# Optimization experiments

Measured on AMD Instinct MI355X. Metric: run time of the kernel, lower is better.

## Reference

```python
import jax, jax.numpy as jnp
import numpy as np

D_MODEL = 1024
NUM_HEADS = 16

def _dense_params(key, d_in, d_out):
    kw, _ = jax.random.split(key)
    # flax default: lecun_normal kernel, zeros bias
    W = jax.random.normal(kw, (d_in, d_out), dtype=jnp.float32) / np.sqrt(d_in)
    b = jnp.zeros((d_out,), dtype=jnp.float32)
    return W, b

def setup_inputs() -> dict:
    key = jax.random.key(0)
    ks = jax.random.split(key, 8)
    B, Tx, Tc = 2, 2048, 2048
    x = jax.random.normal(ks[0], (B, Tx, D_MODEL), dtype=jnp.float32)
    context = jax.random.normal(ks[1], (B, Tc, D_MODEL), dtype=jnp.float32)
    Wq, bq = _dense_params(ks[2], D_MODEL, D_MODEL)
    Wks, bks = _dense_params(ks[3], D_MODEL, D_MODEL)
    Wvs, bvs = _dense_params(ks[4], D_MODEL, D_MODEL)
    Wkc, bkc = _dense_params(ks[5], D_MODEL, D_MODEL)
    Wvc, bvc = _dense_params(ks[6], D_MODEL, D_MODEL)
    Wo, bo = _dense_params(ks[7], D_MODEL, D_MODEL)
    return {"x": x, "context": context,
            "Wq": Wq, "bq": bq, "Wks": Wks, "bks": bks, "Wvs": Wvs, "bvs": bvs,
            "Wkc": Wkc, "bkc": bkc, "Wvc": Wvc, "bvc": bvc, "Wo": Wo, "bo": bo}

def _split_heads(t, H):
    B, T, C = t.shape
    return t.reshape(B, T, H, C // H).transpose(0, 2, 1, 3)  # [B,H,T,hd]

def reference(x, context, Wq, bq, Wks, bks, Wvs, bvs, Wkc, bkc, Wvc, bvc, Wo, bo):
    H = NUM_HEADS
    head_dim = D_MODEL // H
    q = x @ Wq + bq
    k = jnp.concatenate([x @ Wks + bks, context @ Wkc + bkc], axis=1)
    v = jnp.concatenate([x @ Wvs + bvs, context @ Wvc + bvc], axis=1)
    q = _split_heads(q, H)  # [B,H,Tq,hd]
    k = _split_heads(k, H)  # [B,H,Tk,hd]
    v = _split_heads(v, H)
    attn = jnp.einsum('bhqd,bhkd->bhqk', q, k) / jnp.sqrt(jnp.float32(head_dim))
    attn = jax.nn.softmax(attn, axis=-1)
    out = jnp.einsum('bhqk,bhkd->bhqd', attn, v)
    B, _, Tq, _ = out.shape
    out = out.transpose(0, 2, 1, 3).reshape(B, Tq, D_MODEL)
    return out @ Wo + bo
```

## Files before the change

### kernel.cpp

```cpp
#include <hip/hip_runtime.h>
#include <hip/hip_bf16.h>
#include <math.h>


typedef _Float16 f16;
typedef _Float16 f16x8 __attribute__((ext_vector_type(8)));
typedef _Float16 f16x4v __attribute__((ext_vector_type(4)));
typedef float    f32x4 __attribute__((ext_vector_type(4)));

#define MFMA_F16(a, b, c) __builtin_amdgcn_mfma_f32_16x16x32_f16((a), (b), (c), 0, 0, 0)

__device__ __forceinline__ void glds16(const f16* g, f16* l) {
    __builtin_amdgcn_global_load_lds(
        (const __attribute__((address_space(1))) void*)g,
        (__attribute__((address_space(3))) void*)l, 16, 0, 0);
}

__global__ __launch_bounds__(256) void convert_xc(
    const float4* __restrict__ x, const float4* __restrict__ ctx,
    f16x4v* __restrict__ xb, f16x4v* __restrict__ cb)
{
    const int n4 = (2 * 2048 * 1024) / 4;
    int i = blockIdx.x * 256 + threadIdx.x;
    float4 v;
    f16x4v* dst;
    if (i < n4) { v = x[i];        dst = xb + i; }
    else        { v = ctx[i - n4]; dst = cb + (i - n4); }
    f16x4v h = { (f16)v.x, (f16)v.y, (f16)v.z, (f16)v.w };
    *dst = h;
}

__global__ __launch_bounds__(256) void pack_w(
    const float* __restrict__ W0, const float* __restrict__ W1,
    const float* __restrict__ W2, const float* __restrict__ W3,
    const float* __restrict__ W4, const float* __restrict__ W5,
    f16* __restrict__ out)
{
    const float* Ws[6] = { W0, W1, W2, W3, W4, W5 };
    const float* W = Ws[blockIdx.z];
    f16* Wt = out + (size_t)blockIdx.z * (1024 * 1024);

    __shared__ float tile[32][33];
    const int tx = threadIdx.x & 31, ty = threadIdx.x >> 5;
    const int n0 = blockIdx.x * 32, k0 = blockIdx.y * 32;

#pragma unroll
    for (int i = 0; i < 4; ++i) {
        int r = i * 8 + ty;
        tile[r][tx] = W[(size_t)(k0 + r) * 1024 + n0 + tx];
    }
    __syncthreads();
#pragma unroll
    for (int i = 0; i < 4; ++i) {
        int r = i * 8 + ty;
        Wt[(size_t)(n0 + r) * 1024 + k0 + tx] = (f16)tile[tx][r];
    }
}

template <typename OutT>
__device__ __forceinline__ void gemm_128x128(
    const f16* __restrict__ A, const f16* __restrict__ Bt,
    const float* __restrict__ bias, OutT* __restrict__ out,
    int row_stride, int row_off)
{
    __shared__ alignas(16) f16 As[128 * 32];
    __shared__ alignas(16) f16 Bs[128 * 32];

    const int m0 = blockIdx.x * 128, n0 = blockIdx.y * 128;
    const int tid = threadIdx.x;
    const int w = tid >> 6, lane = tid & 63, quad = lane >> 4, l15 = lane & 15;
    const int wm = (w >> 1) * 64, wn = (w & 1) * 64;

    const int r0 = tid >> 2, ch0 = (tid & 3) * 8;
    f16* as0 = &As[(w * 64) * 8];
    f16* as1 = &As[(256 + w * 64) * 8];
    f16* bs0 = &Bs[(w * 64) * 8];
    f16* bs1 = &Bs[(256 + w * 64) * 8];

    f32x4 acc[4][4] = {};

    for (int k0 = 0; k0 < 1024; k0 += 32) {
        glds16(&A[(size_t)(m0 + r0) * 1024 + k0 + ch0], as0);
        glds16(&A[(size_t)(m0 + 64 + r0) * 1024 + k0 + ch0], as1);
        glds16(&Bt[(size_t)(n0 + r0) * 1024 + k0 + ch0], bs0);
        glds16(&Bt[(size_t)(n0 + 64 + r0) * 1024 + k0 + ch0], bs1);
        __syncthreads();

        f16x8 a[4], b[4];
#pragma unroll
        for (int i = 0; i < 4; ++i) a[i] = *(const f16x8*)&As[(wm + i * 16 + l15) * 32 + quad * 8];
#pragma unroll
        for (int i = 0; i < 4; ++i) b[i] = *(const f16x8*)&Bs[(wn + i * 16 + l15) * 32 + quad * 8];

#pragma unroll
        for (int mi = 0; mi < 4; ++mi)
#pragma unroll
            for (int ni = 0; ni < 4; ++ni)
                acc[mi][ni] = MFMA_F16(a[mi], b[ni], acc[mi][ni]);
        __syncthreads();
    }

#pragma unroll
    for (int mi = 0; mi < 4; ++mi) {
#pragma unroll
        for (int r = 0; r < 4; ++r) {
            int row = m0 + wm + mi * 16 + quad * 4 + r;
            int orow = (row >> 11) * row_stride + row_off + (row & 2047);
#pragma unroll
            for (int ni = 0; ni < 4; ++ni) {
                int col = n0 + wn + ni * 16 + l15;
                out[(size_t)orow * 1024 + col] = (OutT)(acc[mi][ni][r] + bias[col]);
            }
        }
    }
}

__global__ __launch_bounds__(256) void proj_gemm(
    const f16* __restrict__ xb, const f16* __restrict__ cb,
    const f16* __restrict__ wt,
    const float* __restrict__ bq, const float* __restrict__ bks,
    const float* __restrict__ bvs, const float* __restrict__ bkc,
    const float* __restrict__ bvc,
    f16* __restrict__ qbuf, f16* __restrict__ kbuf, f16* __restrict__ vbuf)
{
    const int z = blockIdx.z;
    const f16* A = (z <= 2) ? xb : cb;
    const f16* Bt = wt + (size_t)z * (1024 * 1024);
    const float* bias = (z == 0) ? bq : (z == 1) ? bks : (z == 2) ? bvs
                       : (z == 3) ? bkc : bvc;
    f16* out = (z == 0) ? qbuf : (z == 1 || z == 3) ? kbuf : vbuf;
    const int row_stride = (z == 0) ? 2048 : 4096;
    const int row_off = (z >= 3) ? 2048 : 0;
    gemm_128x128<f16>(A, Bt, bias, out, row_stride, row_off);
}

__global__ __launch_bounds__(256) void out_gemm(
    const f16* __restrict__ abuf, const f16* __restrict__ wt_o,
    const float* __restrict__ bo, float* __restrict__ out)
{
    gemm_128x128<float>(abuf, wt_o, bo, out, 2048, 0);
}

__global__ __launch_bounds__(256) void transpose_v(
    const f16* __restrict__ vbuf, f16* __restrict__ vt)
{
    const int t = threadIdx.x;
    const int mt = t >> 3, md = t & 7;
    const int tok0 = blockIdx.x * 256 + mt * 8;
    const int z = blockIdx.y;
    const int b = z >> 4, h = z & 15;
    f16x8 in[8];
#pragma unroll
    for (int i = 0; i < 8; ++i)
        in[i] = *(const f16x8*)&vbuf[(size_t)(b * 4096 + tok0 + i) * 1024 + h * 64 + md * 8];
    f16x8 ov[8];
#pragma unroll
    for (int j = 0; j < 8; ++j)
#pragma unroll
        for (int i = 0; i < 8; ++i) ov[j][i] = in[i][j];
#pragma unroll
    for (int j = 0; j < 8; ++j)
        *(f16x8*)&vt[(size_t)(z * 64 + md * 8 + j) * 4096 + blockIdx.x * 256 + mt * 8] = ov[j];
}

__global__ __launch_bounds__(256) void attn_kernel(
    const f16* __restrict__ q, const f16* __restrict__ k,
    const f16* __restrict__ vt, f16* __restrict__ o)
{
    __shared__ alignas(16) f16 K_lds[2][64][32];
    __shared__ alignas(16) f16 V_lds[2][64][32];
    __shared__ alignas(16) f16 P_lds[4][16][72];

    const int tid = threadIdx.x;
    const int w = tid >> 6, lane = tid & 63, quad = lane >> 4, l15 = lane & 15;
    const int qt = blockIdx.x, h = blockIdx.y, b = blockIdx.z;
    const int qbase = qt * 64;

    const size_t qrow = (size_t)(b * 2048 + qbase + w * 16 + l15);
    const f16x8 qa0 = *(const f16x8*)&q[qrow * 1024 + h * 64 + quad * 8];
    const f16x8 qa1 = *(const f16x8*)&q[qrow * 1024 + h * 64 + 32 + quad * 8];

    f16x8 ones;
#pragma unroll
    for (int j = 0; j < 8; ++j) ones[j] = (f16)1.0f;

    f32x4 o_acc[4] = {};
    f32x4 l_acc = {};

    const size_t kbase  = ((size_t)b * 4096) * 1024 + h * 64;
    const size_t vtbase = ((size_t)(b * 16 + h) * 64) * 4096;

    const int srow = tid >> 2, sch = (tid & 3) * 8;
    f16* kl0 = &K_lds[0][0][0] + w * 512;
    f16* kl1 = &K_lds[1][0][0] + w * 512;
    f16* vl0 = &V_lds[0][0][0] + w * 512;
    f16* vl1 = &V_lds[1][0][0] + w * 512;

    for (int kt = 0; kt < 64; ++kt) {
        __syncthreads();
        glds16(&k[kbase + (size_t)(kt * 64 + srow) * 1024 + sch], kl0);
        glds16(&k[kbase + (size_t)(kt * 64 + srow) * 1024 + 32 + sch], kl1);
        glds16(&vt[vtbase + (size_t)srow * 4096 + kt * 64 + sch], vl0);
        glds16(&vt[vtbase + (size_t)srow * 4096 + kt * 64 + 32 + sch], vl1);
        __syncthreads();

        f32x4 s[4];
#pragma unroll
        for (int nt = 0; nt < 4; ++nt) {
            f16x8 ka0 = *(const f16x8*)&K_lds[0][nt * 16 + l15][quad * 8];
            f16x8 ka1 = *(const f16x8*)&K_lds[1][nt * 16 + l15][quad * 8];
            f32x4 t = {};
            t = MFMA_F16(ka0, qa0, t);
            t = MFMA_F16(ka1, qa1, t);
            s[nt] = t;
        }

#pragma unroll
        for (int nt = 0; nt < 4; ++nt) {
            f16x4v pk;
#pragma unroll
            for (int r = 0; r < 4; ++r)
                pk[r] = (f16)__expf(s[nt][r] * 0.125f - 5.0f);
            *(f16x4v*)&P_lds[w][l15][nt * 16 + quad * 4] = pk;
        }
        __syncthreads();

        const f16x8 pa0 = *(const f16x8*)&P_lds[w][l15][quad * 8];
        const f16x8 pa1 = *(const f16x8*)&P_lds[w][l15][32 + quad * 8];

        l_acc = MFMA_F16(ones, pa0, l_acc);
        l_acc = MFMA_F16(ones, pa1, l_acc);

#pragma unroll
        for (int dt = 0; dt < 4; ++dt) {
            f16x8 vb0 = *(const f16x8*)&V_lds[0][dt * 16 + l15][quad * 8];
            f16x8 vb1 = *(const f16x8*)&V_lds[1][dt * 16 + l15][quad * 8];
            o_acc[dt] = MFMA_F16(pa0, vb0, o_acc[dt]);
            o_acc[dt] = MFMA_F16(pa1, vb1, o_acc[dt]);
        }
    }

#pragma unroll
    for (int r = 0; r < 4; ++r) {
        float lr = __shfl(l_acc[0], quad * 4 + r, 64);
        float inv = 1.0f / lr;
        int row_local = w * 16 + quad * 4 + r;
        size_t obase = ((size_t)(b * 2048 + qbase + row_local)) * 1024 + h * 64;
#pragma unroll
        for (int dt = 0; dt < 4; ++dt)
            o[obase + dt * 16 + l15] = (f16)(o_acc[dt][r] * inv);
    }
}

extern "C" void kernel_launch(void* const* d_in, const int* in_sizes, int n_in,
                              void* d_out, int out_size, void* d_ws, size_t ws_size,
                              hipStream_t stream)
{
    (void)in_sizes; (void)n_in; (void)out_size; (void)ws_size;

    const float* x    = (const float*)d_in[0];
    const float* ctx  = (const float*)d_in[1];
    const float* Wq   = (const float*)d_in[2];  const float* bq  = (const float*)d_in[3];
    const float* Wks  = (const float*)d_in[4];  const float* bks = (const float*)d_in[5];
    const float* Wvs  = (const float*)d_in[6];  const float* bvs = (const float*)d_in[7];
    const float* Wkc  = (const float*)d_in[8];  const float* bkc = (const float*)d_in[9];
    const float* Wvc  = (const float*)d_in[10]; const float* bvc = (const float*)d_in[11];
    const float* Wo   = (const float*)d_in[12]; const float* bo  = (const float*)d_in[13];

    char* ws = (char*)d_ws;
    f16* xb   = (f16*)(ws + 0);
    f16* cb   = (f16*)(ws + 8388608);
    f16* vt   = (f16*)(ws + 0);
    f16* wt   = (f16*)(ws + 16777216);
    f16* qbuf = (f16*)(ws + 29360128);
    f16* kbuf = (f16*)(ws + 37748736);
    f16* vbuf = (f16*)(ws + 54525952);
    f16* abuf = (f16*)(ws + 71303168);

    convert_xc<<<8192, 256, 0, stream>>>((const float4*)x, (const float4*)ctx,
                                         (f16x4v*)xb, (f16x4v*)cb);
    pack_w<<<dim3(32, 32, 6), 256, 0, stream>>>(Wq, Wks, Wvs, Wkc, Wvc, Wo, wt);
    proj_gemm<<<dim3(32, 8, 5), 256, 0, stream>>>(xb, cb, wt, bq, bks, bvs, bkc, bvc,
                                                  qbuf, kbuf, vbuf);
    transpose_v<<<dim3(16, 32), 256, 0, stream>>>(vbuf, vt);
    attn_kernel<<<dim3(32, 16, 2), 256, 0, stream>>>(qbuf, kbuf, vt, abuf);
    out_gemm<<<dim3(32, 8, 1), 256, 0, stream>>>(abuf, wt + 5 * (size_t)(1024 * 1024),
                                                 bo, (float*)d_out);
}
```

Measured before the change: 328.5 us.

## Pre-tile Q/K/V layouts in GEMM epilogue, widen attention and GEMM K tiles

The GEMM becomes a templated kernel that loads 64-wide K slices per iteration and selects its epilogue layout by mode. The Q projection is written head-major with the softmax scale folded in for exp2. K is written in a pre-tiled per-head layout so attention can load whole 128-key tiles with contiguous global-to-LDS copies. Attention now processes 128 keys per iteration with exp2, drops one barrier, and uses a bh-major grid. The output GEMM uses BN=64 so more blocks are launched. All of this aims to cut strided loads, loop and barrier overhead, and launch imbalance, at the cost of higher register and LDS use and more complex indexing.

```diff
diff --git a/kernel.cpp b/kernel.cpp
--- a/kernel.cpp
+++ b/kernel.cpp
@@ -9,6 +9,9 @@
 typedef float    f32x4 __attribute__((ext_vector_type(4)));
 
 #define MFMA_F16(a, b, c) __builtin_amdgcn_mfma_f32_16x16x32_f16((a), (b), (c), 0, 0, 0)
+
+#define QSCALE 0.18033688011112042f
+#define EXPOFF 7.2134752044448170f
 
 __device__ __forceinline__ void glds16(const f16* g, f16* l) {
     __builtin_amdgcn_global_load_lds(
@@ -57,47 +60,71 @@
     }
 }
 
-template <typename OutT>
-__device__ __forceinline__ void gemm_128x128(
-    const f16* __restrict__ A, const f16* __restrict__ Bt,
-    const float* __restrict__ bias, OutT* __restrict__ out,
-    int row_stride, int row_off)
-{
-    __shared__ alignas(16) f16 As[128 * 32];
-    __shared__ alignas(16) f16 Bs[128 * 32];
-
-    const int m0 = blockIdx.x * 128, n0 = blockIdx.y * 128;
+template <int MODE, int BN, typename OutT>
+__global__ __launch_bounds__(256) void gemm_kernel(
+    const f16* __restrict__ A0, const f16* __restrict__ A1,
+    const f16* __restrict__ Wt,
+    const float* __restrict__ bias0, const float* __restrict__ bias1,
+    OutT* __restrict__ out)
+{
+    __shared__ alignas(16) f16 As[2 * 128 * 32];
+    __shared__ alignas(16) f16 Bs[2 * BN * 32];
+
+    const int z = blockIdx.z;
+    const f16* A = z ? A1 : A0;
+    const f16* Bt = Wt + (size_t)z * 2097152;
+    const float* bias = z ? bias1 : bias0;
+    const int roff = z * 2048;
+
+    const int m0 = blockIdx.x * 128, n0 = blockIdx.y * BN;
     const int tid = threadIdx.x;
     const int w = tid >> 6, lane = tid & 63, quad = lane >> 4, l15 = lane & 15;
-    const int wm = (w >> 1) * 64, wn = (w & 1) * 64;
-
-    const int r0 = tid >> 2, ch0 = (tid & 3) * 8;
-    f16* as0 = &As[(w * 64) * 8];
-    f16* as1 = &As[(256 + w * 64) * 8];
-    f16* bs0 = &Bs[(w * 64) * 8];
-    f16* bs1 = &Bs[(256 + w * 64) * 8];
-
-    f32x4 acc[4][4] = {};
-
-    for (int k0 = 0; k0 < 1024; k0 += 32) {
-        glds16(&A[(size_t)(m0 + r0) * 1024 + k0 + ch0], as0);
-        glds16(&A[(size_t)(m0 + 64 + r0) * 1024 + k0 + ch0], as1);
-        glds16(&Bt[(size_t)(n0 + r0) * 1024 + k0 + ch0], bs0);
-        glds16(&Bt[(size_t)(n0 + 64 + r0) * 1024 + k0 + ch0], bs1);
+    const int wm = (w >> 1) * 64, wn = (w & 1) * (BN / 2);
+    constexpr int NF = BN / 32;
+    constexpr int APASS = 4;
+    constexpr int BPASS = BN / 32;
+
+    int gA[APASS], gB[BPASS];
+#pragma unroll
+    for (int p = 0; p < APASS; ++p) {
+        int c = tid + p * 256;
+        gA[p] = (m0 + ((c >> 2) & 127)) * 1024 + (c >> 9) * 32 + (c & 3) * 8;
+    }
+#pragma unroll
+    for (int p = 0; p < BPASS; ++p) {
+        int c = tid + p * 256;
+        gB[p] = (n0 + ((c >> 2) & (BN - 1))) * 1024 + (c / (BN * 4)) * 32 + (c & 3) * 8;
+    }
+    f16* asl = &As[w * 512];
+    f16* bsl = &Bs[w * 512];
+
+    f32x4 acc[4][NF] = {};
+
+    for (int k0 = 0; k0 < 1024; k0 += 64) {
         __syncthreads();
-
-        f16x8 a[4], b[4];
-#pragma unroll
-        for (int i = 0; i < 4; ++i) a[i] = *(const f16x8*)&As[(wm + i * 16 + l15) * 32 + quad * 8];
-#pragma unroll
-        for (int i = 0; i < 4; ++i) b[i] = *(const f16x8*)&Bs[(wn + i * 16 + l15) * 32 + quad * 8];
-
-#pragma unroll
-        for (int mi = 0; mi < 4; ++mi)
-#pragma unroll
-            for (int ni = 0; ni < 4; ++ni)
-                acc[mi][ni] = MFMA_F16(a[mi], b[ni], acc[mi][ni]);
+#pragma unroll
+        for (int p = 0; p < APASS; ++p)
+            glds16(&A[gA[p] + k0], asl + p * 2048);
+#pragma unroll
+        for (int p = 0; p < BPASS; ++p)
+            glds16(&Bt[gB[p] + k0], bsl + p * 2048);
         __syncthreads();
+
+#pragma unroll
+        for (int ks = 0; ks < 2; ++ks) {
+            f16x8 a[4], b[NF];
+#pragma unroll
+            for (int i = 0; i < 4; ++i)
+                a[i] = *(const f16x8*)&As[ks * 4096 + (wm + i * 16 + l15) * 32 + quad * 8];
+#pragma unroll
+            for (int i = 0; i < NF; ++i)
+                b[i] = *(const f16x8*)&Bs[ks * (BN * 32) + (wn + i * 16 + l15) * 32 + quad * 8];
+#pragma unroll
+            for (int mi = 0; mi < 4; ++mi)
+#pragma unroll
+                for (int ni = 0; ni < NF; ++ni)
+                    acc[mi][ni] = MFMA_F16(a[mi], b[ni], acc[mi][ni]);
+        }
     }
 
 #pragma unroll
@@ -105,40 +132,32 @@
 #pragma unroll
         for (int r = 0; r < 4; ++r) {
             int row = m0 + wm + mi * 16 + quad * 4 + r;
-            int orow = (row >> 11) * row_stride + row_off + (row & 2047);
-#pragma unroll
-            for (int ni = 0; ni < 4; ++ni) {
+            int b_ = row >> 11, tok = row & 2047;
+#pragma unroll
+            for (int ni = 0; ni < NF; ++ni) {
                 int col = n0 + wn + ni * 16 + l15;
-                out[(size_t)orow * 1024 + col] = (OutT)(acc[mi][ni][r] + bias[col]);
+                float v = acc[mi][ni][r] + bias[col];
+                size_t addr;
+                if (MODE == 0) {
+                    addr = (size_t)row * 1024 + col;
+                } else if (MODE == 1) {
+                    v *= QSCALE;
+                    int bh = b_ * 16 + (col >> 6);
+                    addr = ((size_t)bh * 2048 + tok) * 64 + (col & 63);
+                } else if (MODE == 2) {
+                    int tg = roff + tok;
+                    int bh = b_ * 16 + (col >> 6);
+                    addr = (size_t)bh * 262144 + (size_t)(tg >> 7) * 8192
+                         + (size_t)((col >> 5) & 1) * 4096 + (tg & 127) * 32 + (col & 31);
+                } else {
+                    int tg = roff + tok;
+                    int bh = b_ * 16 + (col >> 6);
+                    addr = (size_t)bh * 262144 + (size_t)tg * 64 + (col & 63);
+                }
+                out[addr] = (OutT)v;
             }
         }
     }
-}
-
-__global__ __launch_bounds__(256) void proj_gemm(
-    const f16* __restrict__ xb, const f16* __restrict__ cb,
-    const f16* __restrict__ wt,
-    const float* __restrict__ bq, const float* __restrict__ bks,
-    const float* __restrict__ bvs, const float* __restrict__ bkc,
-    const float* __restrict__ bvc,
-    f16* __restrict__ qbuf, f16* __restrict__ kbuf, f16* __restrict__ vbuf)
-{
-    const int z = blockIdx.z;
-    const f16* A = (z <= 2) ? xb : cb;
-    const f16* Bt = wt + (size_t)z * (1024 * 1024);
-    const float* bias = (z == 0) ? bq : (z == 1) ? bks : (z == 2) ? bvs
-                       : (z == 3) ? bkc : bvc;
-    f16* out = (z == 0) ? qbuf : (z == 1 || z == 3) ? kbuf : vbuf;
-    const int row_stride = (z == 0) ? 2048 : 4096;
-    const int row_off = (z >= 3) ? 2048 : 0;
-    gemm_128x128<f16>(A, Bt, bias, out, row_stride, row_off);
-}
-
-__global__ __launch_bounds__(256) void out_gemm(
-    const f16* __restrict__ abuf, const f16* __restrict__ wt_o,
-    const float* __restrict__ bo, float* __restrict__ out)
-{
-    gemm_128x128<float>(abuf, wt_o, bo, out, 2048, 0);
 }
 
 __global__ __launch_bounds__(256) void transpose_v(
@@ -148,37 +167,39 @@
     const int mt = t >> 3, md = t & 7;
     const int tok0 = blockIdx.x * 256 + mt * 8;
     const int z = blockIdx.y;
-    const int b = z >> 4, h = z & 15;
     f16x8 in[8];
 #pragma unroll
     for (int i = 0; i < 8; ++i)
-        in[i] = *(const f16x8*)&vbuf[(size_t)(b * 4096 + tok0 + i) * 1024 + h * 64 + md * 8];
+        in[i] = *(const f16x8*)&vbuf[((size_t)z * 4096 + tok0 + i) * 64 + md * 8];
     f16x8 ov[8];
 #pragma unroll
     for (int j = 0; j < 8; ++j)
 #pragma unroll
         for (int i = 0; i < 8; ++i) ov[j][i] = in[i][j];
+    const int kt = tok0 >> 7, kks = (tok0 >> 5) & 3, kko = tok0 & 31;
 #pragma unroll
     for (int j = 0; j < 8; ++j)
-        *(f16x8*)&vt[(size_t)(z * 64 + md * 8 + j) * 4096 + blockIdx.x * 256 + mt * 8] = ov[j];
+        *(f16x8*)&vt[(size_t)z * 262144 + (size_t)kt * 8192 + kks * 2048
+                     + (md * 8 + j) * 32 + kko] = ov[j];
 }
 
 __global__ __launch_bounds__(256) void attn_kernel(
-    const f16* __restrict__ q, const f16* __restrict__ k,
-    const f16* __restrict__ vt, f16* __restrict__ o)
-{
-    __shared__ alignas(16) f16 K_lds[2][64][32];
-    __shared__ alignas(16) f16 V_lds[2][64][32];
-    __shared__ alignas(16) f16 P_lds[4][16][72];
+    const f16* __restrict__ q, const f16* __restrict__ kb,
+    const f16* __restrict__ vtb, f16* __restrict__ o)
+{
+    __shared__ alignas(16) f16 K_lds[8192];
+    __shared__ alignas(16) f16 V_lds[8192];
+    __shared__ alignas(16) f16 P_lds[4][16][136];
 
     const int tid = threadIdx.x;
     const int w = tid >> 6, lane = tid & 63, quad = lane >> 4, l15 = lane & 15;
-    const int qt = blockIdx.x, h = blockIdx.y, b = blockIdx.z;
+    const int bh = blockIdx.x, qt = blockIdx.y;
+    const int b = bh >> 4, h = bh & 15;
     const int qbase = qt * 64;
 
-    const size_t qrow = (size_t)(b * 2048 + qbase + w * 16 + l15);
-    const f16x8 qa0 = *(const f16x8*)&q[qrow * 1024 + h * 64 + quad * 8];
-    const f16x8 qa1 = *(const f16x8*)&q[qrow * 1024 + h * 64 + 32 + quad * 8];
+    const size_t qaddr = ((size_t)bh * 2048 + qbase + w * 16 + l15) * 64 + quad * 8;
+    const f16x8 qa0 = *(const f16x8*)&q[qaddr];
+    const f16x8 qa1 = *(const f16x8*)&q[qaddr + 32];
 
     f16x8 ones;
 #pragma unroll
@@ -187,56 +208,58 @@
     f32x4 o_acc[4] = {};
     f32x4 l_acc = {};
 
-    const size_t kbase  = ((size_t)b * 4096) * 1024 + h * 64;
-    const size_t vtbase = ((size_t)(b * 16 + h) * 64) * 4096;
-
-    const int srow = tid >> 2, sch = (tid & 3) * 8;
-    f16* kl0 = &K_lds[0][0][0] + w * 512;
-    f16* kl1 = &K_lds[1][0][0] + w * 512;
-    f16* vl0 = &V_lds[0][0][0] + w * 512;
-    f16* vl1 = &V_lds[1][0][0] + w * 512;
-
-    for (int kt = 0; kt < 64; ++kt) {
+    const f16* ktile = kb + (size_t)bh * 262144;
+    const f16* vtile = vtb + (size_t)bh * 262144;
+    const int coff = tid * 8;
+    f16* kl = &K_lds[w * 512];
+    f16* vl = &V_lds[w * 512];
+
+    for (int kt = 0; kt < 32; ++kt) {
         __syncthreads();
-        glds16(&k[kbase + (size_t)(kt * 64 + srow) * 1024 + sch], kl0);
-        glds16(&k[kbase + (size_t)(kt * 64 + srow) * 1024 + 32 + sch], kl1);
-        glds16(&vt[vtbase + (size_t)srow * 4096 + kt * 64 + sch], vl0);
-        glds16(&vt[vtbase + (size_t)srow * 4096 + kt * 64 + 32 + sch], vl1);
+#pragma unroll
+        for (int p = 0; p < 4; ++p) {
+            glds16(&ktile[coff + p * 2048], kl + p * 2048);
+            glds16(&vtile[coff + p * 2048], vl + p * 2048);
+        }
+        ktile += 8192; vtile += 8192;
         __syncthreads();
 
-        f32x4 s[4];
-#pragma unroll
-        for (int nt = 0; nt < 4; ++nt) {
-            f16x8 ka0 = *(const f16x8*)&K_lds[0][nt * 16 + l15][quad * 8];
-            f16x8 ka1 = *(const f16x8*)&K_lds[1][nt * 16 + l15][quad * 8];
+        f32x4 s[8];
+#pragma unroll
+        for (int mt = 0; mt < 8; ++mt) {
+            f16x8 ka0 = *(const f16x8*)&K_lds[(mt * 16 + l15) * 32 + quad * 8];
+            f16x8 ka1 = *(const f16x8*)&K_lds[4096 + (mt * 16 + l15) * 32 + quad * 8];
             f32x4 t = {};
             t = MFMA_F16(ka0, qa0, t);
             t = MFMA_F16(ka1, qa1, t);
-            s[nt] = t;
-        }
-
-#pragma unroll
-        for (int nt = 0; nt < 4; ++nt) {
+            s[mt] = t;
+        }
+
+#pragma unroll
+        for (int mt = 0; mt < 8; ++mt) {
             f16x4v pk;
 #pragma unroll
             for (int r = 0; r < 4; ++r)
-                pk[r] = (f16)__expf(s[nt][r] * 0.125f - 5.0f);
-            *(f16x4v*)&P_lds[w][l15][nt * 16 + quad * 4] = pk;
-        }
-        __syncthreads();
-
-        const f16x8 pa0 = *(const f16x8*)&P_lds[w][l15][quad * 8];
-        const f16x8 pa1 = *(const f16x8*)&P_lds[w][l15][32 + quad * 8];
-
-        l_acc = MFMA_F16(ones, pa0, l_acc);
-        l_acc = MFMA_F16(ones, pa1, l_acc);
+                pk[r] = (f16)__builtin_amdgcn_exp2f(s[mt][r] - EXPOFF);
+            *(f16x4v*)&P_lds[w][l15][mt * 16 + quad * 4] = pk;
+        }
+
+        f16x8 pa[4];
+#pragma unroll
+        for (int ks = 0; ks < 4; ++ks)
+            pa[ks] = *(const f16x8*)&P_lds[w][l15][ks * 32 + quad * 8];
+
+#pragma unroll
+        for (int ks = 0; ks < 4; ++ks)
+            l_acc = MFMA_F16(ones, pa[ks], l_acc);
 
 #pragma unroll
         for (int dt = 0; dt < 4; ++dt) {
-            f16x8 vb0 = *(const f16x8*)&V_lds[0][dt * 16 + l15][quad * 8];
-            f16x8 vb1 = *(const f16x8*)&V_lds[1][dt * 16 + l15][quad * 8];
-            o_acc[dt] = MFMA_F16(pa0, vb0, o_acc[dt]);
-            o_acc[dt] = MFMA_F16(pa1, vb1, o_acc[dt]);
+#pragma unroll
+            for (int ks = 0; ks < 4; ++ks) {
+                f16x8 vb = *(const f16x8*)&V_lds[ks * 2048 + (dt * 16 + l15) * 32 + quad * 8];
+                o_acc[dt] = MFMA_F16(pa[ks], vb, o_acc[dt]);
+            }
         }
     }
 
@@ -280,10 +303,17 @@
     convert_xc<<<8192, 256, 0, stream>>>((const float4*)x, (const float4*)ctx,
                                          (f16x4v*)xb, (f16x4v*)cb);
     pack_w<<<dim3(32, 32, 6), 256, 0, stream>>>(Wq, Wks, Wvs, Wkc, Wvc, Wo, wt);
-    proj_gemm<<<dim3(32, 8, 5), 256, 0, stream>>>(xb, cb, wt, bq, bks, bvs, bkc, bvc,
-                                                  qbuf, kbuf, vbuf);
+
+    gemm_kernel<1, 128, f16><<<dim3(32, 8, 1), 256, 0, stream>>>(
+        xb, xb, wt, bq, bq, qbuf);
+    gemm_kernel<2, 128, f16><<<dim3(32, 8, 2), 256, 0, stream>>>(
+        xb, cb, wt + 1 * 1048576, bks, bkc, kbuf);
+    gemm_kernel<3, 128, f16><<<dim3(32, 8, 2), 256, 0, stream>>>(
+        xb, cb, wt + 2 * 1048576, bvs, bvc, vbuf);
+
     transpose_v<<<dim3(16, 32), 256, 0, stream>>>(vbuf, vt);
-    attn_kernel<<<dim3(32, 16, 2), 256, 0, stream>>>(qbuf, kbuf, vt, abuf);
-    out_gemm<<<dim3(32, 8, 1), 256, 0, stream>>>(abuf, wt + 5 * (size_t)(1024 * 1024),
-                                                 bo, (float*)d_out);
-}
+    attn_kernel<<<dim3(32, 32), 256, 0, stream>>>(qbuf, kbuf, vt, abuf);
+
+    gemm_kernel<0, 64, float><<<dim3(32, 16, 1), 256, 0, stream>>>(
+        abuf, abuf, wt + 5 * 1048576, bo, bo, (float*)d_out);
+}
```

After: 355.7 us. +8.3%, slower.
